# Performance work log

Measured on AMD Instinct MI355X. Metric: run time of the kernel, lower is better.

Reference implementation:

```python
import jax, jax.numpy as jnp
import numpy as np

B, H, S, D = 2, 16, 2048, 64  # depth = dmodel / num_heads
DMODEL = H * D


def setup_inputs() -> dict:
    key = jax.random.key(0)
    kq, kk, kv, kw = jax.random.split(key, 4)
    Q = jax.random.normal(kq, (B, H, S, D), dtype=jnp.float32)
    K = jax.random.normal(kk, (B, H, S, D), dtype=jnp.float32)
    V = jax.random.normal(kv, (B, H, S, D), dtype=jnp.float32)
    W = jax.random.normal(kw, (DMODEL, DMODEL), dtype=jnp.float32) * (1.0 / np.sqrt(DMODEL))
    b = jnp.zeros((DMODEL,), dtype=jnp.float32)
    return {"Q": Q, "K": K, "V": V, "W": W, "b": b}


def reference(Q, K, V, W, b):
    depth = Q.shape[-1]
    # scores: (B, H, S, S) -- full score matrix, matching the original math
    scores = jnp.einsum('bhqd,bhkd->bhqk', Q, K) / jnp.sqrt(jnp.float32(depth))
    attn = jax.nn.softmax(scores, axis=-1)
    vals = jnp.einsum('bhqk,bhkd->bhqd', attn, V)          # (B, H, S, D)
    vals = jnp.transpose(vals, (0, 2, 1, 3))               # (B, S, H, D)
    concat = vals.reshape(vals.shape[0], vals.shape[1], -1)  # (B, S, dmodel)
    return concat @ W + b
```

## Files before the change

kernel.cpp:

```cpp
#include <hip/hip_runtime.h>
#include <hip/hip_bf16.h>


typedef float  f32x16 __attribute__((ext_vector_type(16)));
typedef float  f32x4v __attribute__((ext_vector_type(4)));
typedef float  f32x2v __attribute__((ext_vector_type(2)));
typedef __bf16 bf16x8 __attribute__((ext_vector_type(8)));
typedef __bf16 bf16x4 __attribute__((ext_vector_type(4)));
typedef __bf16 bf16x2 __attribute__((ext_vector_type(2)));

static constexpr int Bn = 2, Hn = 16, Sn = 2048, Dn = 64, DM = 1024;
static constexpr size_t QKV_ELEMS = (size_t)Bn * Hn * Sn * Dn;

#define QSCALE 0.18033688011112042f

#define LGKM_BARRIER() do {                                  \
    asm volatile("s_waitcnt lgkmcnt(0)" ::: "memory");       \
    __builtin_amdgcn_s_barrier();                            \
  } while (0)

#if __has_builtin(__builtin_amdgcn_cvt_pk_bf16_f32)
static __device__ __forceinline__ unsigned pack2(float a, float b) {
  bf16x2 t = __builtin_amdgcn_cvt_pk_bf16_f32(a, b);
  union { bf16x2 v; unsigned u; } c; c.v = t; return c.u;
}
#else
static __device__ __forceinline__ unsigned pack2(float a, float b) {
  union { __bf16 h; unsigned short s; } ua, ub;
  ua.h = (__bf16)a; ub.h = (__bf16)b;
  return (unsigned)ua.s | ((unsigned)ub.s << 16);
}
#endif

static __device__ __forceinline__ void unzip8(const unsigned* wds, bf16x8* r0, bf16x8* r1) {
  union { unsigned u[4]; bf16x8 v; } a, b;
#pragma unroll
  for (int i = 0; i < 4; ++i) {
    unsigned lo = wds[2 * i], hi = wds[2 * i + 1];
    a.u[i] = (lo & 0xffffu) | (hi << 16);
    b.u[i] = (lo >> 16) | (hi & 0xffff0000u);
  }
  *r0 = a.v; *r1 = b.v;
}

__global__ __launch_bounds__(256) void convert_all(
    const float* __restrict__ k,
    const float* __restrict__ v, const float* __restrict__ w,
    __bf16* __restrict__ ko,
    __bf16* __restrict__ vt, __bf16* __restrict__ wt) {
  __shared__ __bf16 T[64][74];
  const int bid = blockIdx.x, t = threadIdx.x;

  if (bid < 2048) {
    size_t i = ((size_t)bid * 256 + t) * 8;
    f32x4v a = *(const f32x4v*)(k + i);
    f32x4v b = *(const f32x4v*)(k + i + 4);
    bf16x8 o;
#pragma unroll
    for (int j = 0; j < 4; ++j) { o[j] = (__bf16)a[j]; o[4 + j] = (__bf16)b[j]; }
    *(bf16x8*)(ko + i) = o;
    return;
  }

  const float* s0;
  __bf16* dst0;
  size_t dst_stride;
  {
    const int r = t >> 2, c0 = (t & 3) * 16;
    if (bid < 3072) {
      const int idx = bid - 2048;
      const int kv0 = (idx & 31) * 64, bh = idx >> 5;
      s0 = v + ((size_t)bh * Sn + kv0 + r) * Dn + c0;
      dst0 = vt + (size_t)bh * Dn * Sn + kv0;
      dst_stride = Sn;
    } else {
      const int idx = bid - 3072;
      const int nt = (idx & 15) * 64, kt = (idx >> 4) * 64;
      s0 = w + (size_t)(kt + r) * DM + nt + c0;
      dst0 = wt + (size_t)nt * DM + kt;
      dst_stride = DM;
    }
    union { bf16x8 v8; unsigned u[4]; } o0, o1;
#pragma unroll
    for (int i = 0; i < 2; ++i) {
      f32x4v f = *(const f32x4v*)(s0 + i * 4);
#pragma unroll
      for (int j = 0; j < 4; ++j) o0.v8[i * 4 + j] = (__bf16)f[j];
    }
#pragma unroll
    for (int i = 0; i < 2; ++i) {
      f32x4v f = *(const f32x4v*)(s0 + 8 + i * 4);
#pragma unroll
      for (int j = 0; j < 4; ++j) o1.v8[i * 4 + j] = (__bf16)f[j];
    }
#pragma unroll
    for (int j = 0; j < 4; ++j) {
      *(unsigned*)&T[r][c0 + 2 * j]     = o0.u[j];
      *(unsigned*)&T[r][c0 + 8 + 2 * j] = o1.u[j];
    }
  }
  __syncthreads();
  const int rp = t >> 3, k0 = (t & 7) * 8;
  unsigned wds[8];
#pragma unroll
  for (int i = 0; i < 8; ++i) wds[i] = *(const unsigned*)&T[k0 + i][2 * rp];
  bf16x8 r0, r1; unzip8(wds, &r0, &r1);
  __bf16* d0 = dst0 + (size_t)(2 * rp) * dst_stride + k0;
  *(bf16x8*)d0 = r0;
  *(bf16x8*)(d0 + dst_stride) = r1;
}

__global__ __launch_bounds__(256, 4) void attn(
    const float* __restrict__ Qf, const __bf16* __restrict__ Kb,
    const __bf16* __restrict__ Vtg, __bf16* __restrict__ Cc) {
  const int tid = threadIdx.x;
  const int wave = tid >> 6, lane = tid & 63;
  const int ln = lane & 31, g = lane >> 5;
  const int qg = wave >> 1, kh = wave & 1;
  const int qb = blockIdx.x, h = blockIdx.y, bz = blockIdx.z;

  __shared__ __bf16 smem[2][2][64][72];
  __bf16 (*Ks)[64][72] = smem[0];
  __bf16 (*Vs)[64][72] = smem[1];

  const size_t hoff = (size_t)(bz * Hn + h) * Sn * Dn;
  const float*  Qp = Qf + hoff + (size_t)(qb * 64 + qg * 32) * Dn;
  const __bf16* Kp = Kb + hoff;
  const __bf16* Vp = Vtg + hoff;

  bf16x8 qf[4];
#pragma unroll
  for (int ks = 0; ks < 4; ++ks) {
    const float* qp = Qp + (size_t)ln * Dn + ks * 16 + g * 8;
    f32x4v f0 = *(const f32x4v*)qp;
    f32x4v f1 = *(const f32x4v*)(qp + 4);
#pragma unroll
    for (int j = 0; j < 4; ++j) {
      qf[ks][j]     = (__bf16)(f0[j] * QSCALE);
      qf[ks][4 + j] = (__bf16)(f1[j] * QSCALE);
    }
  }

  const int sr = tid >> 2, sc = (tid & 3) * 16;
  const __bf16* kbase = Kp + (size_t)sr * Dn + sc;
  const __bf16* vbase = Vp + (size_t)sr * Sn + sc;

  bf16x8 k0r = *(const bf16x8*)kbase, k1r = *(const bf16x8*)(kbase + 8);
  bf16x8 v0r = *(const bf16x8*)vbase, v1r = *(const bf16x8*)(vbase + 8);
  {
    *(bf16x8*)&Ks[0][sr][sc]     = k0r;
    *(bf16x8*)&Ks[0][sr][sc + 8] = k1r;
    union { bf16x8 v; bf16x4 h[2]; } u0, u1; u0.v = v0r; u1.v = v1r;
    union { bf16x4 h[2]; bf16x8 v; } w0, w1;
    w0.h[0] = u0.h[0]; w0.h[1] = u1.h[0];
    w1.h[0] = u0.h[1]; w1.h[1] = u1.h[1];
    *(bf16x8*)&Vs[0][sr][sc]     = w0.v;
    *(bf16x8*)&Vs[0][sr][sc + 8] = w1.v;
  }
  k0r = *(const bf16x8*)(kbase + (size_t)64 * Dn);
  k1r = *(const bf16x8*)(kbase + (size_t)64 * Dn + 8);
  v0r = *(const bf16x8*)(vbase + 64);
  v1r = *(const bf16x8*)(vbase + 64 + 8);
  LGKM_BARRIER();

  f32x16 O0 = {}, O1 = {};
  float Lown = 0.0f;
  constexpr int NT = Sn / 64;

  for (int kt = 0; kt < NT; ++kt) {
    const int buf = kt & 1;

    bf16x8 kf[4];
#pragma unroll
    for (int ks = 0; ks < 4; ++ks)
      kf[ks] = *(const bf16x8*)&Ks[buf][kh * 32 + ln][ks * 16 + g * 8];

    f32x16 s = {};
    __builtin_amdgcn_s_setprio(1);
#pragma unroll
    for (int ks = 0; ks < 4; ++ks)
      s = __builtin_amdgcn_mfma_f32_32x32x16_bf16(kf[ks], qf[ks], s, 0, 0, 0);
    __builtin_amdgcn_s_setprio(0);

    bf16x8 vf[2][2];
#pragma unroll
    for (int s4 = 0; s4 < 2; ++s4) {
      const int cb = kh * 32 + s4 * 16 + g * 8;
      vf[s4][0] = *(const bf16x8*)&Vs[buf][ln][cb];
      vf[s4][1] = *(const bf16x8*)&Vs[buf][32 + ln][cb];
    }

    if (kt + 1 < NT) {
      const int nb = buf ^ 1;
      *(bf16x8*)&Ks[nb][sr][sc]     = k0r;
      *(bf16x8*)&Ks[nb][sr][sc + 8] = k1r;
      union { bf16x8 v; bf16x4 h[2]; } u0, u1; u0.v = v0r; u1.v = v1r;
      union { bf16x4 h[2]; bf16x8 v; } w0, w1;
      w0.h[0] = u0.h[0]; w0.h[1] = u1.h[0];
      w1.h[0] = u0.h[1]; w1.h[1] = u1.h[1];
      *(bf16x8*)&Vs[nb][sr][sc]     = w0.v;
      *(bf16x8*)&Vs[nb][sr][sc + 8] = w1.v;
      if (kt + 2 < NT) {
        const __bf16* kp = kbase + (size_t)(kt + 2) * 64 * Dn;
        k0r = *(const bf16x8*)kp; k1r = *(const bf16x8*)(kp + 8);
        const __bf16* vp = vbase + (kt + 2) * 64;
        v0r = *(const bf16x8*)vp; v1r = *(const bf16x8*)(vp + 8);
      }
    }

    float p[16];
#pragma unroll
    for (int r = 0; r < 16; ++r) p[r] = __builtin_amdgcn_exp2f(s[r]);
    f32x2v s2 = {0.0f, 0.0f};
#pragma unroll
    for (int tt = 0; tt < 8; ++tt) { f32x2v t2 = {p[2 * tt], p[2 * tt + 1]}; s2 += t2; }
    Lown += s2[0] + s2[1];
    unsigned w[8];
#pragma unroll
    for (int tt = 0; tt < 8; ++tt) w[tt] = pack2(p[2 * tt], p[2 * tt + 1]);

    __builtin_amdgcn_s_setprio(1);
#pragma unroll
    for (int s4 = 0; s4 < 2; ++s4) {
      union { unsigned u[4]; bf16x8 v; } pu;
      pu.u[0] = w[s4 * 4 + 0];
      pu.u[1] = w[s4 * 4 + 1];
      pu.u[2] = w[s4 * 4 + 2];
      pu.u[3] = w[s4 * 4 + 3];
      O0 = __builtin_amdgcn_mfma_f32_32x32x16_bf16(vf[s4][0], pu.v, O0, 0, 0, 0);
      O1 = __builtin_amdgcn_mfma_f32_32x32x16_bf16(vf[s4][1], pu.v, O1, 0, 0, 0);
    }
    __builtin_amdgcn_s_setprio(0);

    LGKM_BARRIER();
  }

  const float Lred = Lown + __shfl_xor(Lown, 32);
  float* Ex = (float*)smem;
  const int slot = (qg * 64 + lane) * 36;
  if (kh == 1) {
#pragma unroll
    for (int i = 0; i < 4; ++i) {
      f32x4v t = {O0[4 * i], O0[4 * i + 1], O0[4 * i + 2], O0[4 * i + 3]};
      *(f32x4v*)&Ex[slot + 4 * i] = t;
    }
#pragma unroll
    for (int i = 0; i < 4; ++i) {
      f32x4v t = {O1[4 * i], O1[4 * i + 1], O1[4 * i + 2], O1[4 * i + 3]};
      *(f32x4v*)&Ex[slot + 16 + 4 * i] = t;
    }
    Ex[slot + 32] = Lred;
  }
  __syncthreads();
  float inv = 0.0f;
  if (kh == 0) {
#pragma unroll
    for (int i = 0; i < 4; ++i) {
      f32x4v t = *(const f32x4v*)&Ex[slot + 4 * i];
#pragma unroll
      for (int c = 0; c < 4; ++c) O0[4 * i + c] += t[c];
    }
#pragma unroll
    for (int i = 0; i < 4; ++i) {
      f32x4v t = *(const f32x4v*)&Ex[slot + 16 + 4 * i];
#pragma unroll
      for (int c = 0; c < 4; ++c) O1[4 * i + c] += t[c];
    }
    inv = 1.0f / (Lred + Ex[slot + 32]);
  }
  __syncthreads();
  __bf16* T = (__bf16*)smem;
  if (kh == 0) {
#pragma unroll
    for (int dh = 0; dh < 2; ++dh) {
#pragma unroll
      for (int a = 0; a < 4; ++a) {
        const f32x16 O = dh ? O1 : O0;
        bf16x4 t4;
#pragma unroll
        for (int c = 0; c < 4; ++c) t4[c] = (__bf16)(O[4 * a + c] * inv);
        *(bf16x4*)&T[(qg * 32 + ln) * 72 + dh * 32 + 8 * a + 4 * g] = t4;
      }
    }
  }
  __syncthreads();
  const int q0 = qb * 64;
#pragma unroll
  for (int i = 0; i < 2; ++i) {
    const int rq = i * 32 + (tid >> 3);
    const int c8 = (tid & 7) * 8;
    bf16x8 o = *(const bf16x8*)&T[rq * 72 + c8];
    size_t base = (((size_t)bz * Sn + q0 + rq) * Hn + h) * Dn + c8;
    *(bf16x8*)&Cc[base] = o;
  }
}

__global__ __launch_bounds__(512, 2) void proj(
    const __bf16* __restrict__ A, const __bf16* __restrict__ Wt,
    const float* __restrict__ bias, float* __restrict__ out) {
  const int tid = threadIdx.x, wave = tid >> 6, lane = tid & 63;
  const int ln = lane & 31, g = lane >> 5;
  const int mq = wave >> 1, nh = wave & 1;
  const int bm = blockIdx.x, bn = blockIdx.y;
  __shared__ __bf16 As[2][128][72];
  __shared__ __bf16 Bs[2][64][72];
  const int ar = tid >> 2, ac = (tid & 3) * 16;
  const int rb = tid >> 3, cb = (tid & 7) * 8;
  f32x16 acc = {};
  const __bf16* Ap = A + (size_t)(bm * 128) * DM;
  const __bf16* Wp = Wt + (size_t)(bn * 64) * DM;

  bf16x8 a0, a1, b0;
  {
    const __bf16* ap = Ap + (size_t)ar * DM + ac;
    a0 = *(const bf16x8*)ap; a1 = *(const bf16x8*)(ap + 8);
    b0 = *(const bf16x8*)(Wp + (size_t)rb * DM + cb);
  }
  *(bf16x8*)&As[0][ar][ac]     = a0;
  *(bf16x8*)&As[0][ar][ac + 8] = a1;
  *(bf16x8*)&Bs[0][rb][cb]     = b0;
  {
    const __bf16* ap = Ap + (size_t)ar * DM + 64 + ac;
    a0 = *(const bf16x8*)ap; a1 = *(const bf16x8*)(ap + 8);
    b0 = *(const bf16x8*)(Wp + (size_t)rb * DM + 64 + cb);
  }
  LGKM_BARRIER();

  constexpr int KT = DM / 64;
  for (int kt = 0; kt < KT; ++kt) {
    const int buf = kt & 1;
    __builtin_amdgcn_s_setprio(1);
#pragma unroll
    for (int ks = 0; ks < 4; ++ks) {
      bf16x8 af = *(const bf16x8*)&As[buf][mq * 32 + ln][ks * 16 + g * 8];
      bf16x8 wf = *(const bf16x8*)&Bs[buf][nh * 32 + ln][ks * 16 + g * 8];
      acc = __builtin_amdgcn_mfma_f32_32x32x16_bf16(af, wf, acc, 0, 0, 0);
    }
    __builtin_amdgcn_s_setprio(0);
    if (kt + 1 < KT) {
      const int nb = buf ^ 1;
      *(bf16x8*)&As[nb][ar][ac]     = a0;
      *(bf16x8*)&As[nb][ar][ac + 8] = a1;
      *(bf16x8*)&Bs[nb][rb][cb]     = b0;
      if (kt + 2 < KT) {
        const __bf16* ap = Ap + (size_t)ar * DM + (kt + 2) * 64 + ac;
        a0 = *(const bf16x8*)ap; a1 = *(const bf16x8*)(ap + 8);
        b0 = *(const bf16x8*)(Wp + (size_t)rb * DM + (kt + 2) * 64 + cb);
      }
    }
    LGKM_BARRIER();
  }
  const float bv = bias[bn * 64 + nh * 32 + ln];
#pragma unroll
  for (int r = 0; r < 16; ++r) {
    int row = bm * 128 + mq * 32 + (r & 3) + 8 * (r >> 2) + 4 * g;
    out[(size_t)row * DM + bn * 64 + nh * 32 + ln] = acc[r] + bv;
  }
}

extern "C" void kernel_launch(void* const* d_in, const int* in_sizes, int n_in,
                              void* d_out, int out_size, void* d_ws, size_t ws_size,
                              hipStream_t stream) {
  const float* Q = (const float*)d_in[0];
  const float* K = (const float*)d_in[1];
  const float* V = (const float*)d_in[2];
  const float* W = (const float*)d_in[3];
  const float* b = (const float*)d_in[4];
  float* out = (float*)d_out;

  __bf16* ws  = (__bf16*)d_ws;
  __bf16* Kb  = ws;
  __bf16* Vtg = Kb + QKV_ELEMS;
  __bf16* Cc  = Vtg + QKV_ELEMS;
  __bf16* Wt  = Cc + QKV_ELEMS;

  convert_all<<<dim3(3328, 1, 1), 256, 0, stream>>>(K, V, W, Kb, Vtg, Wt);
  attn<<<dim3(Sn / 64, Hn, Bn), 256, 0, stream>>>(Q, Kb, Vtg, Cc);
  proj<<<dim3(Bn * Sn / 128, DM / 64, 1), 512, 0, stream>>>(Cc, Wt, b, out);
}
```

Measured before the change: 160.2 us.

## Enlarge attention tiles to 128 queries and 128 keys with 512-thread blocks

The attention kernel now uses 512 threads (8 waves) per block, covering 128 query rows and stepping through keys in 128-wide tiles instead of 64. Each staged K/V tile is reused by twice as many query waves, and the key loop runs half as many iterations and barriers. One __syncthreads in the epilogue is removed by writing the output staging area into the V buffer while the exchange area lives in the K buffer. In exchange the kernel needs more shared memory, launches half as many blocks, and holds more registers per wave (16 packed P words), which may reduce occupancy.

Result: no change. 157.5 us (-1.7%).

```diff
diff --git a/kernel.cpp b/kernel.cpp
--- a/kernel.cpp
+++ b/kernel.cpp
@@ -110,7 +110,7 @@
   *(bf16x8*)(d0 + dst_stride) = r1;
 }
 
-__global__ __launch_bounds__(256, 4) void attn(
+__global__ __launch_bounds__(512, 4) void attn(
     const float* __restrict__ Qf, const __bf16* __restrict__ Kb,
     const __bf16* __restrict__ Vtg, __bf16* __restrict__ Cc) {
   const int tid = threadIdx.x;
@@ -119,12 +119,11 @@
   const int qg = wave >> 1, kh = wave & 1;
   const int qb = blockIdx.x, h = blockIdx.y, bz = blockIdx.z;
 
-  __shared__ __bf16 smem[2][2][64][72];
-  __bf16 (*Ks)[64][72] = smem[0];
-  __bf16 (*Vs)[64][72] = smem[1];
+  __shared__ __bf16 Ks[2][128][72];
+  __shared__ __bf16 Vs[2][64][136];
 
   const size_t hoff = (size_t)(bz * Hn + h) * Sn * Dn;
-  const float*  Qp = Qf + hoff + (size_t)(qb * 64 + qg * 32) * Dn;
+  const float*  Qp = Qf + hoff + (size_t)(qb * 128 + qg * 32) * Dn;
   const __bf16* Kp = Kb + hoff;
   const __bf16* Vp = Vtg + hoff;
 
@@ -141,94 +140,93 @@
     }
   }
 
-  const int sr = tid >> 2, sc = (tid & 3) * 16;
-  const __bf16* kbase = Kp + (size_t)sr * Dn + sc;
-  const __bf16* vbase = Vp + (size_t)sr * Sn + sc;
+  const int kr = tid >> 2, kc = (tid & 3) * 16;
+  const int vr = tid >> 3, vc = (tid & 7) * 16;
+  const __bf16* kbase = Kp + (size_t)kr * Dn + kc;
+  const __bf16* vbase = Vp + (size_t)vr * Sn + vc;
 
   bf16x8 k0r = *(const bf16x8*)kbase, k1r = *(const bf16x8*)(kbase + 8);
   bf16x8 v0r = *(const bf16x8*)vbase, v1r = *(const bf16x8*)(vbase + 8);
   {
-    *(bf16x8*)&Ks[0][sr][sc]     = k0r;
-    *(bf16x8*)&Ks[0][sr][sc + 8] = k1r;
+    *(bf16x8*)&Ks[0][kr][kc]     = k0r;
+    *(bf16x8*)&Ks[0][kr][kc + 8] = k1r;
     union { bf16x8 v; bf16x4 h[2]; } u0, u1; u0.v = v0r; u1.v = v1r;
     union { bf16x4 h[2]; bf16x8 v; } w0, w1;
     w0.h[0] = u0.h[0]; w0.h[1] = u1.h[0];
     w1.h[0] = u0.h[1]; w1.h[1] = u1.h[1];
-    *(bf16x8*)&Vs[0][sr][sc]     = w0.v;
-    *(bf16x8*)&Vs[0][sr][sc + 8] = w1.v;
-  }
-  k0r = *(const bf16x8*)(kbase + (size_t)64 * Dn);
-  k1r = *(const bf16x8*)(kbase + (size_t)64 * Dn + 8);
-  v0r = *(const bf16x8*)(vbase + 64);
-  v1r = *(const bf16x8*)(vbase + 64 + 8);
+    *(bf16x8*)&Vs[0][vr][vc]     = w0.v;
+    *(bf16x8*)&Vs[0][vr][vc + 8] = w1.v;
+  }
+  k0r = *(const bf16x8*)(kbase + (size_t)128 * Dn);
+  k1r = *(const bf16x8*)(kbase + (size_t)128 * Dn + 8);
+  v0r = *(const bf16x8*)(vbase + 128);
+  v1r = *(const bf16x8*)(vbase + 128 + 8);
   LGKM_BARRIER();
 
   f32x16 O0 = {}, O1 = {};
   float Lown = 0.0f;
-  constexpr int NT = Sn / 64;
+  constexpr int NT = Sn / 128;
 
   for (int kt = 0; kt < NT; ++kt) {
     const int buf = kt & 1;
 
-    bf16x8 kf[4];
-#pragma unroll
-    for (int ks = 0; ks < 4; ++ks)
-      kf[ks] = *(const bf16x8*)&Ks[buf][kh * 32 + ln][ks * 16 + g * 8];
-
-    f32x16 s = {};
-    __builtin_amdgcn_s_setprio(1);
-#pragma unroll
-    for (int ks = 0; ks < 4; ++ks)
-      s = __builtin_amdgcn_mfma_f32_32x32x16_bf16(kf[ks], qf[ks], s, 0, 0, 0);
-    __builtin_amdgcn_s_setprio(0);
-
-    bf16x8 vf[2][2];
-#pragma unroll
-    for (int s4 = 0; s4 < 2; ++s4) {
-      const int cb = kh * 32 + s4 * 16 + g * 8;
-      vf[s4][0] = *(const bf16x8*)&Vs[buf][ln][cb];
-      vf[s4][1] = *(const bf16x8*)&Vs[buf][32 + ln][cb];
+    unsigned w[16];
+#pragma unroll
+    for (int m = 0; m < 2; ++m) {
+      bf16x8 kf[4];
+#pragma unroll
+      for (int ks = 0; ks < 4; ++ks)
+        kf[ks] = *(const bf16x8*)&Ks[buf][kh * 64 + m * 32 + ln][ks * 16 + g * 8];
+
+      f32x16 s = {};
+      __builtin_amdgcn_s_setprio(1);
+#pragma unroll
+      for (int ks = 0; ks < 4; ++ks)
+        s = __builtin_amdgcn_mfma_f32_32x32x16_bf16(kf[ks], qf[ks], s, 0, 0, 0);
+      __builtin_amdgcn_s_setprio(0);
+
+      float p[16];
+#pragma unroll
+      for (int r = 0; r < 16; ++r) p[r] = __builtin_amdgcn_exp2f(s[r]);
+      f32x2v s2 = {0.0f, 0.0f};
+#pragma unroll
+      for (int tt = 0; tt < 8; ++tt) { f32x2v t2 = {p[2 * tt], p[2 * tt + 1]}; s2 += t2; }
+      Lown += s2[0] + s2[1];
+#pragma unroll
+      for (int tt = 0; tt < 8; ++tt) w[m * 8 + tt] = pack2(p[2 * tt], p[2 * tt + 1]);
     }
 
     if (kt + 1 < NT) {
       const int nb = buf ^ 1;
-      *(bf16x8*)&Ks[nb][sr][sc]     = k0r;
-      *(bf16x8*)&Ks[nb][sr][sc + 8] = k1r;
+      *(bf16x8*)&Ks[nb][kr][kc]     = k0r;
+      *(bf16x8*)&Ks[nb][kr][kc + 8] = k1r;
       union { bf16x8 v; bf16x4 h[2]; } u0, u1; u0.v = v0r; u1.v = v1r;
       union { bf16x4 h[2]; bf16x8 v; } w0, w1;
       w0.h[0] = u0.h[0]; w0.h[1] = u1.h[0];
       w1.h[0] = u0.h[1]; w1.h[1] = u1.h[1];
-      *(bf16x8*)&Vs[nb][sr][sc]     = w0.v;
-      *(bf16x8*)&Vs[nb][sr][sc + 8] = w1.v;
+      *(bf16x8*)&Vs[nb][vr][vc]     = w0.v;
+      *(bf16x8*)&Vs[nb][vr][vc + 8] = w1.v;
       if (kt + 2 < NT) {
-        const __bf16* kp = kbase + (size_t)(kt + 2) * 64 * Dn;
+        const __bf16* kp = kbase + (size_t)(kt + 2) * 128 * Dn;
         k0r = *(const bf16x8*)kp; k1r = *(const bf16x8*)(kp + 8);
-        const __bf16* vp = vbase + (kt + 2) * 64;
+        const __bf16* vp = vbase + (kt + 2) * 128;
         v0r = *(const bf16x8*)vp; v1r = *(const bf16x8*)(vp + 8);
       }
     }
 
-    float p[16];
-#pragma unroll
-    for (int r = 0; r < 16; ++r) p[r] = __builtin_amdgcn_exp2f(s[r]);
-    f32x2v s2 = {0.0f, 0.0f};
-#pragma unroll
-    for (int tt = 0; tt < 8; ++tt) { f32x2v t2 = {p[2 * tt], p[2 * tt + 1]}; s2 += t2; }
-    Lown += s2[0] + s2[1];
-    unsigned w[8];
-#pragma unroll
-    for (int tt = 0; tt < 8; ++tt) w[tt] = pack2(p[2 * tt], p[2 * tt + 1]);
-
     __builtin_amdgcn_s_setprio(1);
 #pragma unroll
-    for (int s4 = 0; s4 < 2; ++s4) {
+    for (int s4 = 0; s4 < 4; ++s4) {
+      const int cb = kh * 64 + s4 * 16 + g * 8;
+      bf16x8 vf0 = *(const bf16x8*)&Vs[buf][ln][cb];
+      bf16x8 vf1 = *(const bf16x8*)&Vs[buf][32 + ln][cb];
       union { unsigned u[4]; bf16x8 v; } pu;
       pu.u[0] = w[s4 * 4 + 0];
       pu.u[1] = w[s4 * 4 + 1];
       pu.u[2] = w[s4 * 4 + 2];
       pu.u[3] = w[s4 * 4 + 3];
-      O0 = __builtin_amdgcn_mfma_f32_32x32x16_bf16(vf[s4][0], pu.v, O0, 0, 0, 0);
-      O1 = __builtin_amdgcn_mfma_f32_32x32x16_bf16(vf[s4][1], pu.v, O1, 0, 0, 0);
+      O0 = __builtin_amdgcn_mfma_f32_32x32x16_bf16(vf0, pu.v, O0, 0, 0, 0);
+      O1 = __builtin_amdgcn_mfma_f32_32x32x16_bf16(vf1, pu.v, O1, 0, 0, 0);
     }
     __builtin_amdgcn_s_setprio(0);
 
@@ -236,7 +234,7 @@
   }
 
   const float Lred = Lown + __shfl_xor(Lown, 32);
-  float* Ex = (float*)smem;
+  float* Ex = (float*)Ks;
   const int slot = (qg * 64 + lane) * 36;
   if (kh == 1) {
 #pragma unroll
@@ -252,8 +250,9 @@
     Ex[slot + 32] = Lred;
   }
   __syncthreads();
-  float inv = 0.0f;
+  __bf16* T = (__bf16*)Vs;
   if (kh == 0) {
+    float inv;
 #pragma unroll
     for (int i = 0; i < 4; ++i) {
       f32x4v t = *(const f32x4v*)&Ex[slot + 4 * i];
@@ -267,10 +266,6 @@
       for (int c = 0; c < 4; ++c) O1[4 * i + c] += t[c];
     }
     inv = 1.0f / (Lred + Ex[slot + 32]);
-  }
-  __syncthreads();
-  __bf16* T = (__bf16*)smem;
-  if (kh == 0) {
 #pragma unroll
     for (int dh = 0; dh < 2; ++dh) {
 #pragma unroll
@@ -284,10 +279,10 @@
     }
   }
   __syncthreads();
-  const int q0 = qb * 64;
+  const int q0 = qb * 128;
 #pragma unroll
   for (int i = 0; i < 2; ++i) {
-    const int rq = i * 32 + (tid >> 3);
+    const int rq = i * 64 + (tid >> 3);
     const int c8 = (tid & 7) * 8;
     bf16x8 o = *(const bf16x8*)&T[rq * 72 + c8];
     size_t base = (((size_t)bz * Sn + q0 + rq) * Hn + h) * Dn + c8;
@@ -375,6 +370,6 @@
   __bf16* Wt  = Cc + QKV_ELEMS;
 
   convert_all<<<dim3(3328, 1, 1), 256, 0, stream>>>(K, V, W, Kb, Vtg, Wt);
-  attn<<<dim3(Sn / 64, Hn, Bn), 256, 0, stream>>>(Q, Kb, Vtg, Cc);
+  attn<<<dim3(Sn / 128, Hn, Bn), 512, 0, stream>>>(Q, Kb, Vtg, Cc);
   proj<<<dim3(Bn * Sn / 128, DM / 64, 1), 512, 0, stream>>>(Cc, Wt, b, out);
 }
```
